# Kernel optimization log

Hardware: AMD Instinct MI355X
Metric: run time of the kernel (lower is better)

## Reference

```python
import jax, jax.numpy as jnp
import numpy as np
import math

N_STOCKS, SEQ_T, D_FEAT, D_MODEL = 1024, 32, 158, 256
H_T, H_S = 4, 4
MAX_LEN = 100
LN_EPS = 1e-5


def _make_pe():
    # PositionalEncoding buffer, identical to the torch construction
    pos = np.arange(MAX_LEN, dtype=np.float32)[:, None]
    div = np.exp(np.arange(0, D_MODEL, 2, dtype=np.float32) * (-math.log(10000.0) / D_MODEL))
    pe = np.zeros((MAX_LEN, D_MODEL), dtype=np.float32)
    pe[:, 0::2] = np.sin(pos * div)
    pe[:, 1::2] = np.cos(pos * div)
    return jnp.asarray(pe)


def _ln(x, g, b):
    mu = x.mean(-1, keepdims=True)
    var = ((x - mu) ** 2).mean(-1, keepdims=True)
    return (x - mu) / jnp.sqrt(var + LN_EPS) * g + b


def _mha(q, k, v, nhead, scale):
    # q,k,v: [B,S,D]; full (non-causal) attention over S, vectorized over heads
    B, S, D = q.shape
    hd = D // nhead
    qh = q.reshape(B, S, nhead, hd)
    kh = k.reshape(B, S, nhead, hd)
    vh = v.reshape(B, S, nhead, hd)
    scores = jnp.einsum('bqhd,bkhd->bhqk', qh, kh) * scale
    attn = jax.nn.softmax(scores, axis=-1)  # dropout is identity in eval
    out = jnp.einsum('bhqk,bkhd->bqhd', attn, vh)
    return out.reshape(B, S, D)


def _block(x, wq, wk, wv, g1, b1, g2, b2, w1, bb1, w2, bb2, nhead, scale, swap):
    # shared body of TAttention (swap=False, scale=1) / SAttention (swap=True, scale=1/temperature)
    xn = _ln(x, g1, b1)
    q, k, v = xn @ wq, xn @ wk, xn @ wv
    if swap:  # SAttention attends over the stock axis: transpose(0,1)
        q, k, v = q.swapaxes(0, 1), k.swapaxes(0, 1), v.swapaxes(0, 1)
    att = _mha(q, k, v, nhead, scale)
    if swap:
        att = att.swapaxes(0, 1)
    xt = _ln(xn + att, g2, b2)
    ffn = jax.nn.relu(xt @ w1 + bb1) @ w2 + bb2
    return xt + ffn


def _forward(x_enc, emb_w, emb_b, pe,
             t_wq, t_wk, t_wv, t_ln1_g, t_ln1_b, t_ln2_g, t_ln2_b, t_w1, t_b1, t_w2, t_b2,
             s_wq, s_wk, s_wv, s_ln1_g, s_ln1_b, s_ln2_g, s_ln2_b, s_w1, s_b1, s_w2, s_b2,
             ta_w, dec_w, dec_b):
    x = x_enc[0]  # squeeze(dim=0) -> [N, T, d_feat]
    h = x @ emb_w + emb_b + pe[:x.shape[1]]  # embedding + positional encoding
    # TAttention: attention over time axis, NO temperature scaling in source
    h = _block(h, t_wq, t_wk, t_wv, t_ln1_g, t_ln1_b, t_ln2_g, t_ln2_b,
               t_w1, t_b1, t_w2, t_b2, H_T, 1.0, swap=False)
    # SAttention: attention over stock axis, scaled by 1/sqrt(d_model/nhead)
    s_scale = 1.0 / math.sqrt(D_MODEL / H_S)
    h = _block(h, s_wq, s_wk, s_wv, s_ln1_g, s_ln1_b, s_ln2_g, s_ln2_b,
               s_w1, s_b1, s_w2, s_b2, H_S, s_scale, swap=True)
    # TemporalAttention: last-timestep query pooling over T
    hh = h @ ta_w                                  # [N,T,D]
    lam = jnp.einsum('ntd,nd->nt', hh, hh[:, -1, :])
    lam = jax.nn.softmax(lam, axis=1)
    pooled = jnp.einsum('nt,ntd->nd', lam, h)      # matmul(lam[:,None,:], z).squeeze(1)
    return pooled @ dec_w + dec_b                  # [N, 2]


def setup_inputs():
    key = jax.random.key(0)
    ks = iter(jax.random.split(key, 48))
    def w(shape, s=0.02):
        return jax.random.normal(next(ks), shape, dtype=jnp.float32) * s
    D = D_MODEL
    inp = {
        'x_enc': jax.random.normal(next(ks), (1, N_STOCKS, SEQ_T, D_FEAT), jnp.float32),
        'x_mark_enc': jax.random.normal(next(ks), (1, N_STOCKS, SEQ_T, 4), jnp.float32),
        'x_dec': jax.random.normal(next(ks), (1, SEQ_T, D_FEAT), jnp.float32),
        'x_mark_dec': jax.random.normal(next(ks), (1, SEQ_T, 4), jnp.float32),
        'x_tweet': jax.random.randint(next(ks), (1, 128), 0, 30000, dtype=jnp.int32),
        'emb_w': w((D_FEAT, D)), 'emb_b': jnp.zeros((D,), jnp.float32),
        'pe': _make_pe(),
        't_wq': w((D, D)), 't_wk': w((D, D)), 't_wv': w((D, D)),
        't_ln1_g': jnp.ones((D,), jnp.float32), 't_ln1_b': jnp.zeros((D,), jnp.float32),
        't_ln2_g': jnp.ones((D,), jnp.float32), 't_ln2_b': jnp.zeros((D,), jnp.float32),
        't_w1': w((D, D)), 't_b1': jnp.zeros((D,), jnp.float32),
        't_w2': w((D, D)), 't_b2': jnp.zeros((D,), jnp.float32),
        's_wq': w((D, D)), 's_wk': w((D, D)), 's_wv': w((D, D)),
        's_ln1_g': jnp.ones((D,), jnp.float32), 's_ln1_b': jnp.zeros((D,), jnp.float32),
        's_ln2_g': jnp.ones((D,), jnp.float32), 's_ln2_b': jnp.zeros((D,), jnp.float32),
        's_w1': w((D, D)), 's_b1': jnp.zeros((D,), jnp.float32),
        's_w2': w((D, D)), 's_b2': jnp.zeros((D,), jnp.float32),
        'ta_w': w((D, D)),
        'dec_w': w((D, 2)), 'dec_b': jnp.zeros((2,), jnp.float32),
    }
    return inp


def reference(x_enc, x_mark_enc, x_dec, x_mark_dec, x_tweet, emb_w, emb_b, pe,
              t_wq, t_wk, t_wv, t_ln1_g, t_ln1_b, t_ln2_g, t_ln2_b, t_w1, t_b1, t_w2, t_b2,
              s_wq, s_wk, s_wv, s_ln1_g, s_ln1_b, s_ln2_g, s_ln2_b, s_w1, s_b1, s_w2, s_b2,
              ta_w, dec_w, dec_b):
    # x_mark_enc feeds a throwaway fresh Linear whose output is never used;
    # x_dec / x_mark_dec / x_tweet are unused in the source forward.
    pred = _forward(x_enc, emb_w, emb_b, pe,
                    t_wq, t_wk, t_wv, t_ln1_g, t_ln1_b, t_ln2_g, t_ln2_b, t_w1, t_b1, t_w2, t_b2,
                    s_wq, s_wk, s_wv, s_ln1_g, s_ln1_b, s_ln2_g, s_ln2_b, s_w1, s_b1, s_w2, s_b2,
                    ta_w, dec_w, dec_b)
    # (tweet_pred, data_pred, cat_pred, align_loss) all alias data_pred / 0
    return (pred, pred, pred, jnp.float32(0.0))
```

## Files before the change

kernel.cpp:

```cpp
#include <hip/hip_runtime.h>
#include <hip/hip_bf16.h>
#include <math.h>

#define NS 1024
#define ST 32
#define DF 158
#define DM 256
#define KE 192
#define ROWS (NS*ST)
#define SZ ((size_t)ROWS*DM)
#define LN_EPS 1e-5f
#define LOG2E 1.44269504088896f

typedef __attribute__((ext_vector_type(8)))  __bf16 bf16x8;
typedef __attribute__((ext_vector_type(16))) float  f32x16;

__device__ __forceinline__ float wave_sum(float v) {
#pragma unroll
    for (int o = 32; o > 0; o >>= 1) v += __shfl_xor(v, o);
    return v;
}

__device__ __forceinline__ unsigned pkbf(float a, float b) {
    __hip_bfloat16 ha = __float2bfloat16(a), hb = __float2bfloat16(b);
    unsigned short ua, ub;
    __builtin_memcpy(&ua, &ha, 2); __builtin_memcpy(&ub, &hb, 2);
    return (unsigned)ua | ((unsigned)ub << 16);
}

__device__ __forceinline__ unsigned pkbf_fast(float a, float b) {
    unsigned ua = __float_as_uint(a) + 0x8000u;
    unsigned ub = __float_as_uint(b) + 0x8000u;
    return (ua >> 16) | (ub & 0xffff0000u);
}

__device__ __forceinline__ unsigned short sbf(float a) {
    return (unsigned short)((__float_as_uint(a) + 0x8000u) >> 16);
}

__device__ __forceinline__ float2 bf2x(unsigned u) {
    union { unsigned i; float f; } a, b;
    a.i = u << 16; b.i = u & 0xffff0000u;
    return make_float2(a.f, b.f);
}

__device__ __forceinline__ uint4 addpk(uint4 rv, const float* s) {
    float2 f0 = bf2x(rv.x), f1 = bf2x(rv.y), f2 = bf2x(rv.z), f3 = bf2x(rv.w);
    return make_uint4(pkbf_fast(f0.x + s[0], f0.y + s[1]),
                      pkbf_fast(f1.x + s[2], f1.y + s[3]),
                      pkbf_fast(f2.x + s[4], f2.y + s[5]),
                      pkbf_fast(f3.x + s[6], f3.y + s[7]));
}

__device__ __forceinline__ uint4 addbk(uint4 a, uint4 b) {
    float2 a0 = bf2x(a.x), a1 = bf2x(a.y), a2 = bf2x(a.z), a3 = bf2x(a.w);
    float2 b0 = bf2x(b.x), b1 = bf2x(b.y), b2 = bf2x(b.z), b3 = bf2x(b.w);
    return make_uint4(pkbf_fast(a0.x + b0.x, a0.y + b0.y),
                      pkbf_fast(a1.x + b1.x, a1.y + b1.y),
                      pkbf_fast(a2.x + b2.x, a2.y + b2.y),
                      pkbf_fast(a3.x + b3.x, a3.y + b3.y));
}

__global__ __launch_bounds__(256) void cvtx_k(const float* __restrict__ x,
        __hip_bfloat16* __restrict__ xb) {
    int idx = blockIdx.x*256 + threadIdx.x;
    int r = idx / KE, c = idx - r*KE;
    float v = (c < DF) ? x[(size_t)r*DF + c] : 0.f;
    xb[idx] = __float2bfloat16(v);
}

struct WPack { const float* s[11]; __hip_bfloat16* d[11]; };

__global__ __launch_bounds__(256) void cvtw_k(WPack wp) {
    const float* W = wp.s[blockIdx.z];
    __hip_bfloat16* Wt = wp.d[blockIdx.z];
    __shared__ float t[64][65];
    int bi = blockIdx.x*64, bj = blockIdx.y*64;
    int r = threadIdx.x >> 2, c0 = (threadIdx.x & 3) * 16;
#pragma unroll
    for (int i = 0; i < 16; i += 4) {
        float4 v = *(const float4*)(W + (size_t)(bi + r)*DM + bj + c0 + i);
        t[r][c0+i+0] = v.x; t[r][c0+i+1] = v.y;
        t[r][c0+i+2] = v.z; t[r][c0+i+3] = v.w;
    }
    __syncthreads();
    unsigned u[8];
#pragma unroll
    for (int i = 0; i < 8; ++i) u[i] = pkbf(t[c0+2*i][r], t[c0+2*i+1][r]);
    __hip_bfloat16* op = Wt + (size_t)(bj + r)*DM + bi + c0;
    *(uint4*)(op)     = make_uint4(u[0], u[1], u[2], u[3]);
    *(uint4*)(op + 8) = make_uint4(u[4], u[5], u[6], u[7]);
}

__global__ __launch_bounds__(192) void cvte_k(const float* __restrict__ W,
        __hip_bfloat16* __restrict__ Wt) {
    int n = blockIdx.x, t = threadIdx.x;
    float v = (t < DF) ? W[(size_t)t*DM + n] : 0.f;
    Wt[(size_t)n*KE + t] = __float2bfloat16(v);
}

__global__ __launch_bounds__(256) void ln_k(const __hip_bfloat16* __restrict__ a,
        const float* __restrict__ g, const float* __restrict__ be,
        __hip_bfloat16* __restrict__ outb) {
    int w = threadIdx.x >> 6, lane = threadIdx.x & 63;
    size_t r = (size_t)blockIdx.x*4 + w;
    uint2 raw = *(const uint2*)(a + r*DM + lane*4);
    float2 v01 = bf2x(raw.x), v23 = bf2x(raw.y);
    float mu = wave_sum(v01.x+v01.y+v23.x+v23.y) * (1.0f/DM);
    float c0 = v01.x-mu, c1 = v01.y-mu, c2 = v23.x-mu, c3 = v23.y-mu;
    float var = wave_sum(c0*c0 + c1*c1 + c2*c2 + c3*c3) * (1.0f/DM);
    float rs = rsqrtf(var + LN_EPS);
    float4 g4 = *(const float4*)(g + lane*4);
    float4 b4 = *(const float4*)(be + lane*4);
    float o0 = c0*rs*g4.x + b4.x, o1 = c1*rs*g4.y + b4.y;
    float o2 = c2*rs*g4.z + b4.z, o3 = c3*rs*g4.w + b4.w;
    *(uint2*)(outb + r*DM + lane*4) = make_uint2(pkbf_fast(o0, o1), pkbf_fast(o2, o3));
}

union __align__(16) GLds {
    struct { __hip_bfloat16 As[64*72]; __hip_bfloat16 Ws[128*72]; } s;
    __hip_bfloat16 Ob[64*136];
};

__global__ __launch_bounds__(256) void mgemm_k(const __hip_bfloat16* __restrict__ A,
        int sA, int nk, const __hip_bfloat16* __restrict__ Wt, int sW,
        const float* __restrict__ bias, const float* __restrict__ pe,
        const __hip_bfloat16* __restrict__ resid, float* __restrict__ Cf,
        __hip_bfloat16* __restrict__ Cb, int relu, int fmt, float scale, int fused) {
    __shared__ GLds gsm;
    const int tid = threadIdx.x;
    const int w = tid >> 6, lane = tid & 63;
    const int uh = lane >> 5, l31 = lane & 31;
    const int wm = (w >> 1)*32, wn = (w & 1)*64;
    const size_t m0 = (size_t)blockIdx.x*64;
    const int n0 = blockIdx.y*128;

    f32x16 acc[2];
#pragma unroll
    for (int nt = 0; nt < 2; ++nt)
#pragma unroll
        for (int r = 0; r < 16; ++r) acc[nt][r] = 0.f;

    const int ra = tid >> 2, ca = (tid & 3)*16;
    const int rw = tid >> 1, cw = (tid & 1)*32;
    const __hip_bfloat16* ap = A  + (m0 + ra)*sA + ca;
    const __hip_bfloat16* wp = Wt + (size_t)(n0 + rw)*sW + cw;
    uint4 pa0 = *(const uint4*)(ap), pa1 = *(const uint4*)(ap + 8);
    uint4 pw0 = *(const uint4*)(wp),      pw1 = *(const uint4*)(wp + 8);
    uint4 pw2 = *(const uint4*)(wp + 16), pw3 = *(const uint4*)(wp + 24);
    for (int kt = 0; kt < nk; ++kt) {
        __syncthreads();
        *(uint4*)&gsm.s.As[ra*72 + ca]     = pa0;
        *(uint4*)&gsm.s.As[ra*72 + ca + 8] = pa1;
        *(uint4*)&gsm.s.Ws[rw*72 + cw]      = pw0;
        *(uint4*)&gsm.s.Ws[rw*72 + cw + 8]  = pw1;
        *(uint4*)&gsm.s.Ws[rw*72 + cw + 16] = pw2;
        *(uint4*)&gsm.s.Ws[rw*72 + cw + 24] = pw3;
        __syncthreads();
        if (kt + 1 < nk) {
            int ko = (kt + 1)*64;
            pa0 = *(const uint4*)(ap + ko);      pa1 = *(const uint4*)(ap + ko + 8);
            pw0 = *(const uint4*)(wp + ko);      pw1 = *(const uint4*)(wp + ko + 8);
            pw2 = *(const uint4*)(wp + ko + 16); pw3 = *(const uint4*)(wp + ko + 24);
        }
#pragma unroll
        for (int ks = 0; ks < 4; ++ks) {
            bf16x8 a0 = *(const bf16x8*)&gsm.s.As[(wm + l31)*72      + ks*16 + uh*8];
            bf16x8 b0 = *(const bf16x8*)&gsm.s.Ws[(wn + l31)*72      + ks*16 + uh*8];
            bf16x8 b1 = *(const bf16x8*)&gsm.s.Ws[(wn + 32 + l31)*72 + ks*16 + uh*8];
            acc[0] = __builtin_amdgcn_mfma_f32_32x32x16_bf16(a0, b0, acc[0], 0, 0, 0);
            acc[1] = __builtin_amdgcn_mfma_f32_32x32x16_bf16(a0, b1, acc[1], 0, 0, 0);
        }
    }

    if (Cf) {
#pragma unroll
        for (int nt = 0; nt < 2; ++nt) {
            int colg = n0 + wn + nt*32 + l31;
            float bz = bias ? bias[colg] : 0.f;
#pragma unroll
            for (int r = 0; r < 16; ++r) {
                size_t mg = m0 + wm + (r & 3) + ((r >> 2) << 3) + 4*uh;
                float v = (acc[nt][r] + bz) * scale;
                if (pe)   v += pe[(mg & 31)*DM + colg];
                if (relu) v = fmaxf(v, 0.f);
                Cf[mg*DM + colg] = v;
            }
        }
    } else {
        __syncthreads();
#pragma unroll
        for (int nt = 0; nt < 2; ++nt) {
            int col = wn + nt*32 + l31;
            int colg = n0 + col;
            int c8  = fused ? (colg & 255) : colg;
            float sc = (fused && (colg >> 8)) ? 1.0f : scale;
            float bz = bias ? bias[c8] : 0.f;
#pragma unroll
            for (int r = 0; r < 16; ++r) {
                int mrow = wm + (r & 3) + ((r >> 2) << 3) + 4*uh;
                float v = (acc[nt][r] + bz) * sc;
                if (pe)   v += pe[((m0 + mrow) & 31)*DM + c8];
                if (relu) v = fmaxf(v, 0.f);
                *(unsigned short*)&gsm.Ob[mrow*136 + col] = sbf(v);
            }
        }
        __syncthreads();
        int m = tid >> 2;
        size_t mg = m0 + m;
#pragma unroll
        for (int i = 0; i < 4; ++i) {
            int ncol = ((tid & 3) + 4*i)*8;
            uint4 val = *(const uint4*)&gsm.Ob[m*136 + ncol];
            int colg = n0 + ncol;
            int seg = fused ? (colg >> 8) : 0;
            int c8  = fused ? (colg & 255) : colg;
            if (resid) val = addbk(val, *(const uint4*)(resid + mg*DM + c8));
            size_t oidx;
            if (fmt == 1)
                oidx = (size_t)((mg & 31)*4 + (c8 >> 6))*65536 + (mg >> 5)*64 + (c8 & 63);
            else if (fmt == 2)
                oidx = ((size_t)(c8 >> 6)*NS + (mg >> 5))*2048 + (mg & 31)*64 + (c8 & 63);
            else
                oidx = mg*DM + c8;
            *(uint4*)&(Cb + (size_t)seg*SZ)[oidx] = val;
        }
    }
}

union __align__(16) WLds { __hip_bfloat16 vt[64*40]; float ob[32*68]; };

__global__ __launch_bounds__(256) void attnT_k(const __hip_bfloat16* __restrict__ Q,
        const __hip_bfloat16* __restrict__ K, const __hip_bfloat16* __restrict__ V,
        const __hip_bfloat16* __restrict__ R, const float* __restrict__ g,
        const float* __restrict__ be, __hip_bfloat16* __restrict__ O) {
    __shared__ WLds sm4[4];
    __shared__ float redS[32][8];
    __shared__ float redQ[32][8];
    const int n = blockIdx.x;
    const int w = threadIdx.x >> 6, lane = threadIdx.x & 63;
    const int uh = lane >> 5, l31 = lane & 31;
    const size_t base = ((size_t)w*NS + n)*2048;

    bf16x8 kf[4], qf[4];
#pragma unroll
    for (int s = 0; s < 4; ++s) {
        kf[s] = *(const bf16x8*)(K + base + l31*64 + s*16 + uh*8);
        qf[s] = *(const bf16x8*)(Q + base + l31*64 + s*16 + uh*8);
    }
    __hip_bfloat16* vt = sm4[w].vt;
#pragma unroll
    for (int i = 0; i < 2; ++i) {
        int c = lane*2 + i;
        int dg = c >> 3, tg = c & 7;
        const ushort* vp = (const ushort*)(V + base + (tg*4)*64 + dg*4);
        ushort4 s0 = *(const ushort4*)(vp);
        ushort4 s1 = *(const ushort4*)(vp + 64);
        ushort4 s2 = *(const ushort4*)(vp + 128);
        ushort4 s3 = *(const ushort4*)(vp + 192);
        *(uint2*)&vt[(dg*4+0)*40 + tg*4] = make_uint2((unsigned)s0.x | ((unsigned)s1.x<<16),
                                                      (unsigned)s2.x | ((unsigned)s3.x<<16));
        *(uint2*)&vt[(dg*4+1)*40 + tg*4] = make_uint2((unsigned)s0.y | ((unsigned)s1.y<<16),
                                                      (unsigned)s2.y | ((unsigned)s3.y<<16));
        *(uint2*)&vt[(dg*4+2)*40 + tg*4] = make_uint2((unsigned)s0.z | ((unsigned)s1.z<<16),
                                                      (unsigned)s2.z | ((unsigned)s3.z<<16));
        *(uint2*)&vt[(dg*4+3)*40 + tg*4] = make_uint2((unsigned)s0.w | ((unsigned)s1.w<<16),
                                                      (unsigned)s2.w | ((unsigned)s3.w<<16));
    }

    f32x16 sa;
#pragma unroll
    for (int r = 0; r < 16; ++r) sa[r] = 0.f;
    sa = __builtin_amdgcn_mfma_f32_32x32x16_bf16(kf[0], qf[0], sa, 0, 0, 0);
    sa = __builtin_amdgcn_mfma_f32_32x32x16_bf16(kf[1], qf[1], sa, 0, 0, 0);
    sa = __builtin_amdgcn_mfma_f32_32x32x16_bf16(kf[2], qf[2], sa, 0, 0, 0);
    sa = __builtin_amdgcn_mfma_f32_32x32x16_bf16(kf[3], qf[3], sa, 0, 0, 0);

    float p[16], l = 0.f;
#pragma unroll
    for (int r = 0; r < 16; ++r) { p[r] = __builtin_amdgcn_exp2f(sa[r]); l += p[r]; }
    l += __shfl_xor(l, 32);

    bf16x8 pf[2];
#pragma unroll
    for (int s = 0; s < 2; ++s) {
        unsigned A0 = pkbf_fast(p[8*s+0], p[8*s+1]);
        unsigned A1 = pkbf_fast(p[8*s+2], p[8*s+3]);
        unsigned B0 = pkbf_fast(p[8*s+4], p[8*s+5]);
        unsigned B1 = pkbf_fast(p[8*s+6], p[8*s+7]);
        unsigned xA0 = (unsigned)__shfl_xor((int)A0, 32);
        unsigned xA1 = (unsigned)__shfl_xor((int)A1, 32);
        unsigned xB0 = (unsigned)__shfl_xor((int)B0, 32);
        unsigned xB1 = (unsigned)__shfl_xor((int)B1, 32);
        union { uint4 i; bf16x8 v; } cv;
        cv.i = make_uint4(uh ? xB0 : A0, uh ? xB1 : A1,
                          uh ? B0 : xA0, uh ? B1 : xA1);
        pf[s] = cv.v;
    }

    f32x16 oa[2];
#pragma unroll
    for (int c = 0; c < 2; ++c) {
#pragma unroll
        for (int r = 0; r < 16; ++r) oa[c][r] = 0.f;
        bf16x8 v0 = *(const bf16x8*)&vt[(c*32 + l31)*40 + uh*8];
        bf16x8 v1 = *(const bf16x8*)&vt[(c*32 + l31)*40 + 16 + uh*8];
        oa[c] = __builtin_amdgcn_mfma_f32_32x32x16_bf16(v0, pf[0], oa[c], 0, 0, 0);
        oa[c] = __builtin_amdgcn_mfma_f32_32x32x16_bf16(v1, pf[1], oa[c], 0, 0, 0);
    }

    float invl = 1.0f / l;
    float* ob = sm4[w].ob;
#pragma unroll
    for (int c = 0; c < 2; ++c)
#pragma unroll
        for (int r = 0; r < 16; ++r) {
            int d = (r & 3) + ((r >> 2) << 3) + 4*uh + 32*c;
            ob[l31*68 + d] = oa[c][r] * invl;
        }
    int t = lane >> 1, d0 = (lane & 1)*32;
    size_t gi = ((size_t)n*ST + t)*DM + w*64 + d0;
    float ps = 0.f, pq = 0.f;
#pragma unroll
    for (int i = 0; i < 4; ++i) {
        uint4 rv = *(const uint4*)(R + gi + 8*i);
        float* s = &ob[t*68 + d0 + 8*i];
        float2 f0 = bf2x(rv.x), f1 = bf2x(rv.y), f2 = bf2x(rv.z), f3 = bf2x(rv.w);
        float v0 = f0.x + s[0], v1 = f0.y + s[1], v2 = f1.x + s[2], v3 = f1.y + s[3];
        float v4 = f2.x + s[4], v5 = f2.y + s[5], v6 = f3.x + s[6], v7 = f3.y + s[7];
        s[0] = v0; s[1] = v1; s[2] = v2; s[3] = v3;
        s[4] = v4; s[5] = v5; s[6] = v6; s[7] = v7;
        ps += v0+v1+v2+v3+v4+v5+v6+v7;
        pq += v0*v0+v1*v1+v2*v2+v3*v3+v4*v4+v5*v5+v6*v6+v7*v7;
    }
    redS[t][w*2 + (lane & 1)] = ps;
    redQ[t][w*2 + (lane & 1)] = pq;
    __syncthreads();
    float s8 = 0.f, q8 = 0.f;
#pragma unroll
    for (int i = 0; i < 8; ++i) { s8 += redS[t][i]; q8 += redQ[t][i]; }
    float mu = s8*(1.0f/DM);
    float var = q8*(1.0f/DM) - mu*mu;
    float rcp = rsqrtf(var + LN_EPS);
#pragma unroll
    for (int i = 0; i < 4; ++i) {
        const float* s = &ob[t*68 + d0 + 8*i];
        int cg = w*64 + d0 + 8*i;
        float4 g0 = *(const float4*)(g + cg),     float4g1 = *(const float4*)(g + cg + 4);
        float4 b0 = *(const float4*)(be + cg),    b1 = *(const float4*)(be + cg + 4);
        float o0 = (s[0]-mu)*rcp*g0.x + b0.x, o1 = (s[1]-mu)*rcp*g0.y + b0.y;
        float o2 = (s[2]-mu)*rcp*g0.z + b0.z, o3 = (s[3]-mu)*rcp*g0.w + b0.w;
        float o4 = (s[4]-mu)*rcp*float4g1.x + b1.x, o5 = (s[5]-mu)*rcp*float4g1.y + b1.y;
        float o6 = (s[6]-mu)*rcp*float4g1.z + b1.z, o7 = (s[7]-mu)*rcp*float4g1.w + b1.w;
        *(uint4*)(O + gi + 8*i) = make_uint4(pkbf_fast(o0, o1), pkbf_fast(o2, o3),
                                             pkbf_fast(o4, o5), pkbf_fast(o6, o7));
    }
}

union __align__(16) LdsS {
    struct { __hip_bfloat16 K[64*72]; __hip_bfloat16 Vt[64*72]; } s;
    float Ob[4][32*68];
};

__global__ __launch_bounds__(256) void attnS_k(const __hip_bfloat16* __restrict__ Qb,
        const __hip_bfloat16* __restrict__ Kb, const __hip_bfloat16* __restrict__ Vb,
        const __hip_bfloat16* __restrict__ R, __hip_bfloat16* __restrict__ O) {
    __shared__ LdsS sm;
    const int tt = blockIdx.x, h = blockIdx.y, qt = blockIdx.z;
    const int tid = threadIdx.x;
    const int w = tid >> 6, lane = tid & 63;
    const int uh = lane >> 5, l31 = lane & 31;
    const size_t hb = (size_t)(tt*4 + h)*65536;

    bf16x8 qf[4];
    {
        const __hip_bfloat16* qp = Qb + hb + (size_t)(qt*128 + w*32 + l31)*64 + 8*uh;
        qf[0] = *(const bf16x8*)(qp);
        qf[1] = *(const bf16x8*)(qp + 16);
        qf[2] = *(const bf16x8*)(qp + 32);
        qf[3] = *(const bf16x8*)(qp + 48);
    }

    f32x16 oa[2];
#pragma unroll
    for (int c = 0; c < 2; ++c)
#pragma unroll
        for (int r = 0; r < 16; ++r) oa[c][r] = 0.f;
    float lrun = 0.f;

    for (int kt = 0; kt < 16; ++kt) {
        __syncthreads();
        {
            const __hip_bfloat16* kb = Kb + hb + (size_t)kt*4096;
#pragma unroll
            for (int i = 0; i < 2; ++i) {
                int c = tid*2 + i;
                int j = c >> 3, col = (c & 7)*8;
                *(uint4*)&sm.s.K[j*72 + col] = *(const uint4*)(kb + c*8);
            }
        }
        {
            int j0 = (tid & 15)*4, cb = (tid >> 4)*4;
            const ushort* vp = (const ushort*)(Vb + hb + (size_t)(kt*64 + j0)*64 + cb);
            ushort4 s0 = *(const ushort4*)(vp);
            ushort4 s1 = *(const ushort4*)(vp + 64);
            ushort4 s2 = *(const ushort4*)(vp + 128);
            ushort4 s3 = *(const ushort4*)(vp + 192);
            *(uint2*)&sm.s.Vt[(cb+0)*72 + j0] = make_uint2((unsigned)s0.x | ((unsigned)s1.x<<16),
                                                           (unsigned)s2.x | ((unsigned)s3.x<<16));
            *(uint2*)&sm.s.Vt[(cb+1)*72 + j0] = make_uint2((unsigned)s0.y | ((unsigned)s1.y<<16),
                                                           (unsigned)s2.y | ((unsigned)s3.y<<16));
            *(uint2*)&sm.s.Vt[(cb+2)*72 + j0] = make_uint2((unsigned)s0.z | ((unsigned)s1.z<<16),
                                                           (unsigned)s2.z | ((unsigned)s3.z<<16));
            *(uint2*)&sm.s.Vt[(cb+3)*72 + j0] = make_uint2((unsigned)s0.w | ((unsigned)s1.w<<16),
                                                           (unsigned)s2.w | ((unsigned)s3.w<<16));
        }
        __syncthreads();

        f32x16 sa[2];
#pragma unroll
        for (int ct = 0; ct < 2; ++ct) {
            f32x16 a2;
#pragma unroll
            for (int r = 0; r < 16; ++r) a2[r] = 0.f;
            const __hip_bfloat16* kb = &sm.s.K[(ct*32 + l31)*72 + 8*uh];
            a2 = __builtin_amdgcn_mfma_f32_32x32x16_bf16(*(const bf16x8*)(kb +  0), qf[0], a2, 0, 0, 0);
            a2 = __builtin_amdgcn_mfma_f32_32x32x16_bf16(*(const bf16x8*)(kb + 16), qf[1], a2, 0, 0, 0);
            a2 = __builtin_amdgcn_mfma_f32_32x32x16_bf16(*(const bf16x8*)(kb + 32), qf[2], a2, 0, 0, 0);
            a2 = __builtin_amdgcn_mfma_f32_32x32x16_bf16(*(const bf16x8*)(kb + 48), qf[3], a2, 0, 0, 0);
            sa[ct] = a2;
        }

        float p[32];
        float rs = 0.f;
#pragma unroll
        for (int ct = 0; ct < 2; ++ct)
#pragma unroll
            for (int r = 0; r < 16; ++r) {
                float e = __builtin_amdgcn_exp2f(sa[ct][r]);
                p[ct*16 + r] = e;
                rs += e;
            }
        rs += __shfl_xor(rs, 32);
        lrun += rs;

        bf16x8 bfr[4];
#pragma unroll
        for (int q = 0; q < 4; ++q) {
            int ct = q >> 1, b = (q & 1) << 3;
            unsigned A0 = pkbf_fast(p[ct*16+b+0], p[ct*16+b+1]);
            unsigned A1 = pkbf_fast(p[ct*16+b+2], p[ct*16+b+3]);
            unsigned B0 = pkbf_fast(p[ct*16+b+4], p[ct*16+b+5]);
            unsigned B1 = pkbf_fast(p[ct*16+b+6], p[ct*16+b+7]);
            unsigned xA0 = (unsigned)__shfl_xor((int)A0, 32);
            unsigned xA1 = (unsigned)__shfl_xor((int)A1, 32);
            unsigned xB0 = (unsigned)__shfl_xor((int)B0, 32);
            unsigned xB1 = (unsigned)__shfl_xor((int)B1, 32);
            union { uint4 i; bf16x8 v; } cv;
            cv.i = make_uint4(uh ? xB0 : A0, uh ? xB1 : A1,
                              uh ? B0 : xA0, uh ? B1 : xA1);
            bfr[q] = cv.v;
        }

#pragma unroll
        for (int c = 0; c < 2; ++c) {
            const __hip_bfloat16* vb = &sm.s.Vt[(c*32 + l31)*72 + 8*uh];
            oa[c] = __builtin_amdgcn_mfma_f32_32x32x16_bf16(*(const bf16x8*)(vb +  0), bfr[0], oa[c], 0, 0, 0);
            oa[c] = __builtin_amdgcn_mfma_f32_32x32x16_bf16(*(const bf16x8*)(vb + 16), bfr[1], oa[c], 0, 0, 0);
            oa[c] = __builtin_amdgcn_mfma_f32_32x32x16_bf16(*(const bf16x8*)(vb + 32), bfr[2], oa[c], 0, 0, 0);
            oa[c] = __builtin_amdgcn_mfma_f32_32x32x16_bf16(*(const bf16x8*)(vb + 48), bfr[3], oa[c], 0, 0, 0);
        }
    }

    __syncthreads();
    float invl = 1.0f / lrun;
    float* ob = sm.Ob[w];
#pragma unroll
    for (int c = 0; c < 2; ++c)
#pragma unroll
        for (int r = 0; r < 16; ++r) {
            int d = (r & 3) + ((r >> 2) << 3) + 4*uh + 32*c;
            ob[l31*68 + d] = oa[c][r] * invl;
        }
#pragma unroll
    for (int pp = 0; pp < 2; ++pp) {
        int qr = pp*16 + (lane >> 2);
        int dc = (lane & 3) << 4;
        size_t gi = ((size_t)(qt*128 + w*32 + qr)*ST + tt)*DM + h*64 + dc;
#pragma unroll
        for (int i = 0; i < 2; ++i) {
            uint4 rv = *(const uint4*)(R + gi + 8*i);
            *(uint4*)(O + gi + 8*i) = addpk(rv, &ob[qr*68 + dc + 8*i]);
        }
    }
}

__global__ __launch_bounds__(256) void final_k(const __hip_bfloat16* __restrict__ H,
        const float* __restrict__ HH, const float* __restrict__ dw,
        const float* __restrict__ db, float* __restrict__ out) {
    int n = blockIdx.x, d = threadIdx.x;
    int w = d >> 6, lane = d & 63;
    __shared__ float lam[ST];
    __shared__ float red[8];
    const float* hh = HH + (size_t)n*ST*DM;
    float4 qd = *(const float4*)(hh + 31*DM + lane*4);
#pragma unroll
    for (int i = 0; i < 8; ++i) {
        int t = w*8 + i;
        float4 h4 = *(const float4*)(hh + t*DM + lane*4);
        float s = wave_sum(h4.x*qd.x + h4.y*qd.y + h4.z*qd.z + h4.w*qd.w);
        if (lane == 0) lam[t] = s;
    }
    __syncthreads();
    float mx = -1e30f;
#pragma unroll
    for (int t = 0; t < ST; ++t) mx = fmaxf(mx, lam[t]);
    float sum = 0.f;
#pragma unroll
    for (int t = 0; t < ST; ++t) sum += __expf(lam[t]-mx);
    float acc = 0.f;
    const __hip_bfloat16* hrow = H + (size_t)n*ST*DM;
#pragma unroll
    for (int t = 0; t < ST; ++t)
        acc += __expf(lam[t]-mx) * __bfloat162float(hrow[t*DM + d]);
    acc /= sum;
    float p0 = wave_sum(acc * dw[2*d+0]);
    float p1 = wave_sum(acc * dw[2*d+1]);
    if (lane == 0) { red[w] = p0; red[4 + w] = p1; }
    __syncthreads();
    if (d == 0) {
        float r0 = red[0]+red[1]+red[2]+red[3] + db[0];
        float r1 = red[4]+red[5]+red[6]+red[7] + db[1];
        out[(size_t)n*2+0] = r0;           out[(size_t)n*2+1] = r1;
        out[2048 + (size_t)n*2+0] = r0;    out[2048 + (size_t)n*2+1] = r1;
        out[4096 + (size_t)n*2+0] = r0;    out[4096 + (size_t)n*2+1] = r1;
        if (n == 0) out[6144] = 0.f;
    }
}

extern "C" void kernel_launch(void* const* d_in, const int* in_sizes, int n_in,
                              void* d_out, int out_size, void* d_ws, size_t ws_size,
                              hipStream_t stream) {
    const float* x     = (const float*)d_in[0];
    const float* emb_w = (const float*)d_in[5];
    const float* emb_b = (const float*)d_in[6];
    const float* pe    = (const float*)d_in[7];
    const float* t_g1  = (const float*)d_in[11];
    const float* t_b1  = (const float*)d_in[12];
    const float* t_g2  = (const float*)d_in[13];
    const float* t_b2  = (const float*)d_in[14];
    const float* t_bb1 = (const float*)d_in[16];
    const float* t_bb2 = (const float*)d_in[18];
    const float* s_g1  = (const float*)d_in[22];
    const float* s_b1  = (const float*)d_in[23];
    const float* s_g2  = (const float*)d_in[24];
    const float* s_b2  = (const float*)d_in[25];
    const float* s_bb1 = (const float*)d_in[27];
    const float* s_bb2 = (const float*)d_in[29];
    const float* dec_w = (const float*)d_in[31];
    const float* dec_b = (const float*)d_in[32];
    float* out = (float*)d_out;

    float* F0 = (float*)d_ws;
    __hip_bfloat16* B0 = (__hip_bfloat16*)(F0 + SZ);
    __hip_bfloat16* B1 = B0 + SZ;
    __hip_bfloat16* B2 = B1 + SZ;
    __hip_bfloat16* B3 = B2 + SZ;
    __hip_bfloat16* B4 = B3 + SZ;
    __hip_bfloat16* WT  = B4 + SZ;
    __hip_bfloat16* WTE = WT + (size_t)11*DM*DM;
    __hip_bfloat16* XB  = WTE + (size_t)DM*KE;

    cvtx_k<<<ROWS*KE/256, 256, 0, stream>>>(x, XB);
    WPack wp;
    const int widx[11] = {8, 9, 10, 15, 17, 19, 20, 21, 26, 28, 30};
    for (int i = 0; i < 11; ++i) {
        wp.s[i] = (const float*)d_in[widx[i]];
        wp.d[i] = WT + (size_t)i*DM*DM;
    }
    cvtw_k<<<dim3(4, 4, 11), 256, 0, stream>>>(wp);
    cvte_k<<<DM, 192, 0, stream>>>(emb_w, WTE);

    dim3 gg(ROWS/64, 2);
    dim3 gq(ROWS/64, 6);
    __hip_bfloat16* WqT = WT;
    __hip_bfloat16* W1  = WT + (size_t)3*DM*DM;
    __hip_bfloat16* W2  = WT + (size_t)4*DM*DM;
    __hip_bfloat16* SWq = WT + (size_t)5*DM*DM;
    __hip_bfloat16* SW1 = WT + (size_t)8*DM*DM;
    __hip_bfloat16* SW2 = WT + (size_t)9*DM*DM;
    __hip_bfloat16* WTA = WT + (size_t)10*DM*DM;

    mgemm_k<<<gg, 256, 0, stream>>>(XB, KE, 3, WTE, KE, emb_b, pe, nullptr, nullptr, B0, 0, 0, 1.f, 0);
    ln_k<<<ROWS/4, 256, 0, stream>>>(B0, t_g1, t_b1, B1);
    mgemm_k<<<gq, 256, 0, stream>>>(B1, 256, 4, WqT, 256, nullptr, nullptr, nullptr, nullptr, B2, 0, 2, LOG2E, 1);
    attnT_k<<<NS, 256, 0, stream>>>(B2, B3, B4, B1, t_g2, t_b2, B1);
    mgemm_k<<<gg, 256, 0, stream>>>(B1, 256, 4, W1, 256, t_bb1, nullptr, nullptr, nullptr, B2, 1, 0, 1.f, 0);
    mgemm_k<<<gg, 256, 0, stream>>>(B2, 256, 4, W2, 256, t_bb2, nullptr, B1, nullptr, B0, 0, 0, 1.f, 0);
    ln_k<<<ROWS/4, 256, 0, stream>>>(B0, s_g1, s_b1, B1);
    mgemm_k<<<gq, 256, 0, stream>>>(B1, 256, 4, SWq, 256, nullptr, nullptr, nullptr, nullptr, B2, 0, 1, 0.125f*LOG2E, 1);
    attnS_k<<<dim3(32, 4, 8), 256, 0, stream>>>(B2, B3, B4, B1, B0);
    ln_k<<<ROWS/4, 256, 0, stream>>>(B0, s_g2, s_b2, B1);
    mgemm_k<<<gg, 256, 0, stream>>>(B1, 256, 4, SW1, 256, s_bb1, nullptr, nullptr, nullptr, B2, 1, 0, 1.f, 0);
    mgemm_k<<<gg, 256, 0, stream>>>(B2, 256, 4, SW2, 256, s_bb2, nullptr, B1, nullptr, B0, 0, 0, 1.f, 0);
    mgemm_k<<<gg, 256, 0, stream>>>(B0, 256, 4, WTA, 256, nullptr, nullptr, nullptr, F0, nullptr, 0, 0, 1.f, 0);
    final_k<<<NS, 256, 0, stream>>>(B0, F0, dec_w, dec_b, out);
}
```

Before: 384.4 us.

## Double-buffer K/V tiles in stock-axis attention and use 2D grid for input cast

The stock-axis attention kernel now keeps two LDS buffers for K and transposed V. The next tile's global loads are issued into registers before the current tile's MFMAs and written to the other buffer afterwards, so each iteration needs one barrier instead of two and load latency can overlap compute. The input conversion kernel switches to a 2D grid so it no longer needs an integer divide per element. In exchange, LDS use per block grows, which may lower occupancy, and more registers stay live across the loop.

```diff
diff --git a/kernel.cpp b/kernel.cpp
--- a/kernel.cpp
+++ b/kernel.cpp
@@ -63,10 +63,10 @@
 
 __global__ __launch_bounds__(256) void cvtx_k(const float* __restrict__ x,
         __hip_bfloat16* __restrict__ xb) {
-    int idx = blockIdx.x*256 + threadIdx.x;
-    int r = idx / KE, c = idx - r*KE;
+    int r = blockIdx.x*8 + (threadIdx.x >> 5);
+    int c = blockIdx.y*32 + (threadIdx.x & 31);
     float v = (c < DF) ? x[(size_t)r*DF + c] : 0.f;
-    xb[idx] = __float2bfloat16(v);
+    xb[(size_t)r*KE + c] = __float2bfloat16(v);
 }
 
 struct WPack { const float* s[11]; __hip_bfloat16* d[11]; };
@@ -346,19 +346,19 @@
     for (int i = 0; i < 4; ++i) {
         const float* s = &ob[t*68 + d0 + 8*i];
         int cg = w*64 + d0 + 8*i;
-        float4 g0 = *(const float4*)(g + cg),     float4g1 = *(const float4*)(g + cg + 4);
-        float4 b0 = *(const float4*)(be + cg),    b1 = *(const float4*)(be + cg + 4);
+        float4 g0 = *(const float4*)(g + cg),  g1 = *(const float4*)(g + cg + 4);
+        float4 b0 = *(const float4*)(be + cg), b1 = *(const float4*)(be + cg + 4);
         float o0 = (s[0]-mu)*rcp*g0.x + b0.x, o1 = (s[1]-mu)*rcp*g0.y + b0.y;
         float o2 = (s[2]-mu)*rcp*g0.z + b0.z, o3 = (s[3]-mu)*rcp*g0.w + b0.w;
-        float o4 = (s[4]-mu)*rcp*float4g1.x + b1.x, o5 = (s[5]-mu)*rcp*float4g1.y + b1.y;
-        float o6 = (s[6]-mu)*rcp*float4g1.z + b1.z, o7 = (s[7]-mu)*rcp*float4g1.w + b1.w;
+        float o4 = (s[4]-mu)*rcp*g1.x + b1.x, o5 = (s[5]-mu)*rcp*g1.y + b1.y;
+        float o6 = (s[6]-mu)*rcp*g1.z + b1.z, o7 = (s[7]-mu)*rcp*g1.w + b1.w;
         *(uint4*)(O + gi + 8*i) = make_uint4(pkbf_fast(o0, o1), pkbf_fast(o2, o3),
                                              pkbf_fast(o4, o5), pkbf_fast(o6, o7));
     }
 }
 
 union __align__(16) LdsS {
-    struct { __hip_bfloat16 K[64*72]; __hip_bfloat16 Vt[64*72]; } s;
+    struct { __hip_bfloat16 K[2][64*72]; __hip_bfloat16 Vt[2][64*72]; } s;
     float Ob[4][32*68];
 };
 
@@ -381,6 +381,32 @@
         qf[3] = *(const bf16x8*)(qp + 48);
     }
 
+    const int kj = tid >> 2, kcol = (tid & 3)*16;
+    const int j0 = (tid & 15)*4, cb = (tid >> 4)*4;
+    const __hip_bfloat16* kbase = Kb + hb;
+    const ushort* vbase = (const ushort*)(Vb + hb);
+    uint4 kr0, kr1; ushort4 vr0, vr1, vr2, vr3;
+
+#define LOADKV(KT) { \
+        const __hip_bfloat16* kb_ = kbase + (size_t)(KT)*4096 + kj*64 + kcol; \
+        kr0 = *(const uint4*)(kb_); kr1 = *(const uint4*)(kb_ + 8); \
+        const ushort* vp_ = vbase + (size_t)((KT)*64 + j0)*64 + cb; \
+        vr0 = *(const ushort4*)(vp_);       vr1 = *(const ushort4*)(vp_ + 64); \
+        vr2 = *(const ushort4*)(vp_ + 128); vr3 = *(const ushort4*)(vp_ + 192); }
+
+#define STOREKV(B) { \
+        __hip_bfloat16* Kd_ = sm.s.K[B]; __hip_bfloat16* Vd_ = sm.s.Vt[B]; \
+        *(uint4*)&Kd_[kj*72 + kcol]     = kr0; \
+        *(uint4*)&Kd_[kj*72 + kcol + 8] = kr1; \
+        *(uint2*)&Vd_[(cb+0)*72 + j0] = make_uint2((unsigned)vr0.x | ((unsigned)vr1.x<<16), \
+                                                   (unsigned)vr2.x | ((unsigned)vr3.x<<16)); \
+        *(uint2*)&Vd_[(cb+1)*72 + j0] = make_uint2((unsigned)vr0.y | ((unsigned)vr1.y<<16), \
+                                                   (unsigned)vr2.y | ((unsigned)vr3.y<<16)); \
+        *(uint2*)&Vd_[(cb+2)*72 + j0] = make_uint2((unsigned)vr0.z | ((unsigned)vr1.z<<16), \
+                                                   (unsigned)vr2.z | ((unsigned)vr3.z<<16)); \
+        *(uint2*)&Vd_[(cb+3)*72 + j0] = make_uint2((unsigned)vr0.w | ((unsigned)vr1.w<<16), \
+                                                   (unsigned)vr2.w | ((unsigned)vr3.w<<16)); }
+
     f32x16 oa[2];
 #pragma unroll
     for (int c = 0; c < 2; ++c)
@@ -388,34 +414,12 @@
         for (int r = 0; r < 16; ++r) oa[c][r] = 0.f;
     float lrun = 0.f;
 
+    LOADKV(0); STOREKV(0);
+    __syncthreads();
+
     for (int kt = 0; kt < 16; ++kt) {
-        __syncthreads();
-        {
-            const __hip_bfloat16* kb = Kb + hb + (size_t)kt*4096;
-#pragma unroll
-            for (int i = 0; i < 2; ++i) {
-                int c = tid*2 + i;
-                int j = c >> 3, col = (c & 7)*8;
-                *(uint4*)&sm.s.K[j*72 + col] = *(const uint4*)(kb + c*8);
-            }
-        }
-        {
-            int j0 = (tid & 15)*4, cb = (tid >> 4)*4;
-            const ushort* vp = (const ushort*)(Vb + hb + (size_t)(kt*64 + j0)*64 + cb);
-            ushort4 s0 = *(const ushort4*)(vp);
-            ushort4 s1 = *(const ushort4*)(vp + 64);
-            ushort4 s2 = *(const ushort4*)(vp + 128);
-            ushort4 s3 = *(const ushort4*)(vp + 192);
-            *(uint2*)&sm.s.Vt[(cb+0)*72 + j0] = make_uint2((unsigned)s0.x | ((unsigned)s1.x<<16),
-                                                           (unsigned)s2.x | ((unsigned)s3.x<<16));
-            *(uint2*)&sm.s.Vt[(cb+1)*72 + j0] = make_uint2((unsigned)s0.y | ((unsigned)s1.y<<16),
-                                                           (unsigned)s2.y | ((unsigned)s3.y<<16));
-            *(uint2*)&sm.s.Vt[(cb+2)*72 + j0] = make_uint2((unsigned)s0.z | ((unsigned)s1.z<<16),
-                                                           (unsigned)s2.z | ((unsigned)s3.z<<16));
-            *(uint2*)&sm.s.Vt[(cb+3)*72 + j0] = make_uint2((unsigned)s0.w | ((unsigned)s1.w<<16),
-                                                           (unsigned)s2.w | ((unsigned)s3.w<<16));
-        }
-        __syncthreads();
+        const int cur = kt & 1;
+        if (kt < 15) LOADKV(kt + 1);
 
         f32x16 sa[2];
 #pragma unroll
@@ -423,7 +427,7 @@
             f32x16 a2;
 #pragma unroll
             for (int r = 0; r < 16; ++r) a2[r] = 0.f;
-            const __hip_bfloat16* kb = &sm.s.K[(ct*32 + l31)*72 + 8*uh];
+            const __hip_bfloat16* kb = &sm.s.K[cur][(ct*32 + l31)*72 + 8*uh];
             a2 = __builtin_amdgcn_mfma_f32_32x32x16_bf16(*(const bf16x8*)(kb +  0), qf[0], a2, 0, 0, 0);
             a2 = __builtin_amdgcn_mfma_f32_32x32x16_bf16(*(const bf16x8*)(kb + 16), qf[1], a2, 0, 0, 0);
             a2 = __builtin_amdgcn_mfma_f32_32x32x16_bf16(*(const bf16x8*)(kb + 32), qf[2], a2, 0, 0, 0);
@@ -432,17 +436,17 @@
         }
 
         float p[32];
-        float rs = 0.f;
+        float rsum = 0.f;
 #pragma unroll
         for (int ct = 0; ct < 2; ++ct)
 #pragma unroll
             for (int r = 0; r < 16; ++r) {
                 float e = __builtin_amdgcn_exp2f(sa[ct][r]);
                 p[ct*16 + r] = e;
-                rs += e;
+                rsum += e;
             }
-        rs += __shfl_xor(rs, 32);
-        lrun += rs;
+        rsum += __shfl_xor(rsum, 32);
+        lrun += rsum;
 
         bf16x8 bfr[4];
 #pragma unroll
@@ -464,15 +468,19 @@
 
 #pragma unroll
         for (int c = 0; c < 2; ++c) {
-            const __hip_bfloat16* vb = &sm.s.Vt[(c*32 + l31)*72 + 8*uh];
+            const __hip_bfloat16* vb = &sm.s.Vt[cur][(c*32 + l31)*72 + 8*uh];
             oa[c] = __builtin_amdgcn_mfma_f32_32x32x16_bf16(*(const bf16x8*)(vb +  0), bfr[0], oa[c], 0, 0, 0);
             oa[c] = __builtin_amdgcn_mfma_f32_32x32x16_bf16(*(const bf16x8*)(vb + 16), bfr[1], oa[c], 0, 0, 0);
             oa[c] = __builtin_amdgcn_mfma_f32_32x32x16_bf16(*(const bf16x8*)(vb + 32), bfr[2], oa[c], 0, 0, 0);
             oa[c] = __builtin_amdgcn_mfma_f32_32x32x16_bf16(*(const bf16x8*)(vb + 48), bfr[3], oa[c], 0, 0, 0);
         }
-    }
-
-    __syncthreads();
+
+        if (kt < 15) STOREKV(cur ^ 1);
+        __syncthreads();
+    }
+#undef LOADKV
+#undef STOREKV
+
     float invl = 1.0f / lrun;
     float* ob = sm.Ob[w];
 #pragma unroll
@@ -571,7 +579,7 @@
     __hip_bfloat16* WTE = WT + (size_t)11*DM*DM;
     __hip_bfloat16* XB  = WTE + (size_t)DM*KE;
 
-    cvtx_k<<<ROWS*KE/256, 256, 0, stream>>>(x, XB);
+    cvtx_k<<<dim3(ROWS/8, KE/32), 256, 0, stream>>>(x, XB);
     WPack wp;
     const int widx[11] = {8, 9, 10, 15, 17, 19, 20, 21, 26, 28, 30};
     for (int i = 0; i < 11; ++i) {
```

Result: no change. 390.1 us (+1.5%).
